# Optimization experiments

Measured on AMD Instinct MI355X. Metric: run time of the kernel, lower is better.

## Reference

```python
import jax, jax.numpy as jnp
import numpy as np

N_NODES = 50000
N_EDGES = 800000
IN_CH = 1024
OUT_CH = 256


def setup_inputs() -> dict:
    key = jax.random.key(0)
    ks = jax.random.split(key, 7)
    x = jax.random.normal(ks[0], (N_NODES, IN_CH), dtype=jnp.float32)
    src_index = jax.random.randint(ks[1], (N_EDGES,), 0, N_NODES, dtype=jnp.int32)
    tar_index = jax.random.randint(ks[2], (N_EDGES,), 0, N_NODES, dtype=jnp.int32)
    edge_weight = jax.random.uniform(ks[3], (N_EDGES,), dtype=jnp.float32)
    self_edge_weight = jax.random.uniform(ks[4], (N_NODES,), dtype=jnp.float32)
    # Linear layer params (torch.nn.Linear: y = x @ W.T + b)
    bound = 1.0 / np.sqrt(IN_CH)
    W = jax.random.uniform(ks[5], (OUT_CH, IN_CH), dtype=jnp.float32, minval=-bound, maxval=bound)
    b = jax.random.uniform(ks[6], (OUT_CH,), dtype=jnp.float32, minval=-bound, maxval=bound)
    return {"x": x, "W": W, "b": b, "src_index": src_index, "tar_index": tar_index,
            "edge_weight": edge_weight, "self_edge_weight": self_edge_weight}


def reference(x, W, b, src_index, tar_index, edge_weight, self_edge_weight):
    # dense linear projection: [N, in] -> [N, out]
    h = jnp.einsum('ni,oi->no', x, W) + b
    # edge aggregation: out[t] += w_e * h[src_e]  (SpMM-like gather/scatter)
    msgs = h[src_index] * edge_weight[:, None]          # [E, out]
    agg = jax.ops.segment_sum(msgs, tar_index, num_segments=h.shape[0])
    # self-loop term
    return agg + self_edge_weight[:, None] * h
```

## Files before the change

### kernel.cpp

```cpp
#include <hip/hip_runtime.h>
#include <hip/hip_bf16.h>

#define N_NODES 50000
#define N_EDGES 800000
#define IN_CH 1024
#define OUT_CH 256
#define NBLK 196

typedef __attribute__((ext_vector_type(8))) short bf16x8;
typedef __attribute__((ext_vector_type(4))) float f32x4;

__device__ inline unsigned short f2bf(float f) {
  union { float f; unsigned int u; } v; v.f = f;
  unsigned int r = v.u + 0x7fffu + ((v.u >> 16) & 1u);
  return (unsigned short)(r >> 16);
}
__device__ inline float bf2f(unsigned short u) {
  union { unsigned int u; float f; } v; v.u = ((unsigned int)u) << 16;
  return v.f;
}
__device__ inline unsigned int cvtpk_bf16(float a, float b) {
  unsigned int r;
  asm("v_cvt_pk_bf16_f32 %0, %1, %2" : "=v"(r) : "v"(a), "v"(b));
  return r;
}

__global__ __launch_bounds__(256) void prep_hist(const float* __restrict__ W,
                                                 unsigned short* __restrict__ Wb,
                                                 const int* __restrict__ tar,
                                                 int* __restrict__ counts) {
  const int b = blockIdx.x, t = threadIdx.x;
  if (b < 256) {
    const int i4 = (b * 256 + t) * 4;
    float4 f = *(const float4*)(W + i4);
    *(ushort4*)(Wb + i4) = make_ushort4(f2bf(f.x), f2bf(f.y), f2bf(f.z), f2bf(f.w));
  } else {
    const int e = (b - 256) * 256 + t;
    if (e < N_EDGES) atomicAdd(&counts[tar[e]], 1);
  }
}

__global__ __launch_bounds__(256, 3) void gemm_proj(
    const float* __restrict__ X, const unsigned short* __restrict__ Wb,
    const float* __restrict__ bias, unsigned short* __restrict__ Hb)
{
  __shared__ unsigned short lds_a[2][64][32];
  __shared__ unsigned short lds_b[2][128][32];

  const int tid  = threadIdx.x;
  const int lane = tid & 63;
  const int w    = tid >> 6;
  const int wr   = w >> 1, wc = w & 1;
  const int gm0  = blockIdx.x * 64;
  const int gn0  = blockIdx.y * 128;

  const int ar = tid >> 3;
  const int ac = (tid & 7) * 4;
  const int br = tid >> 2;
  const int bc = (tid & 3) * 8;

  const int arow0 = gm0 + ar, arow1 = gm0 + ar + 32;
  const bool aok0 = arow0 < N_NODES, aok1 = arow1 < N_NODES;
  const float* xp0 = X + (size_t)arow0 * IN_CH + ac;
  const float* xp1 = X + (size_t)arow1 * IN_CH + ac;
  const unsigned short* wp0 = Wb + (size_t)(gn0 + br) * IN_CH + bc;
  const unsigned short* wp1 = Wb + (size_t)(gn0 + br + 64) * IN_CH + bc;

  f32x4 acc[2][4];
  #pragma unroll
  for (int i = 0; i < 2; i++)
    #pragma unroll
    for (int j = 0; j < 4; j++) acc[i][j] = (f32x4)0.0f;

  float4 pa[3][2];
  bf16x8 pb[2][2];

#define LOADA(KS, SL)                                                          \
  {                                                                            \
    const int k0_ = (KS) * 32;                                                 \
    pa[SL][0] = aok0 ? *(const float4*)(xp0 + k0_)                             \
                     : make_float4(0.f, 0.f, 0.f, 0.f);                        \
    pa[SL][1] = aok1 ? *(const float4*)(xp1 + k0_)                             \
                     : make_float4(0.f, 0.f, 0.f, 0.f);                        \
  }
#define LOADB(KS, SL)                                                          \
  {                                                                            \
    const int k0_ = (KS) * 32;                                                 \
    pb[SL][0] = *(const bf16x8*)(wp0 + k0_);                                   \
    pb[SL][1] = *(const bf16x8*)(wp1 + k0_);                                   \
  }
#define WRITER(BUF, SA, SB)                                                    \
  {                                                                            \
    *(uint2*)&lds_a[BUF][ar][ac] =                                             \
        make_uint2(cvtpk_bf16(pa[SA][0].x, pa[SA][0].y),                       \
                   cvtpk_bf16(pa[SA][0].z, pa[SA][0].w));                      \
    *(uint2*)&lds_a[BUF][ar + 32][ac] =                                        \
        make_uint2(cvtpk_bf16(pa[SA][1].x, pa[SA][1].y),                       \
                   cvtpk_bf16(pa[SA][1].z, pa[SA][1].w));                      \
    *(bf16x8*)&lds_b[BUF][br][bc]      = pb[SB][0];                            \
    *(bf16x8*)&lds_b[BUF][br + 64][bc] = pb[SB][1];                            \
  }
#define COMPUTE(BUF)                                                           \
  {                                                                            \
    const int l15_ = lane & 15;                                                \
    const int kb_  = (lane >> 4) * 8;                                          \
    bf16x8 a0 = *(const bf16x8*)&lds_a[BUF][wr * 32 + l15_][kb_];              \
    bf16x8 a1 = *(const bf16x8*)&lds_a[BUF][wr * 32 + 16 + l15_][kb_];         \
    bf16x8 b0 = *(const bf16x8*)&lds_b[BUF][wc * 64 + l15_][kb_];              \
    bf16x8 b1 = *(const bf16x8*)&lds_b[BUF][wc * 64 + 16 + l15_][kb_];         \
    bf16x8 b2 = *(const bf16x8*)&lds_b[BUF][wc * 64 + 32 + l15_][kb_];         \
    bf16x8 b3 = *(const bf16x8*)&lds_b[BUF][wc * 64 + 48 + l15_][kb_];         \
    acc[0][0] = __builtin_amdgcn_mfma_f32_16x16x32_bf16(a0, b0, acc[0][0], 0, 0, 0); \
    acc[0][1] = __builtin_amdgcn_mfma_f32_16x16x32_bf16(a0, b1, acc[0][1], 0, 0, 0); \
    acc[0][2] = __builtin_amdgcn_mfma_f32_16x16x32_bf16(a0, b2, acc[0][2], 0, 0, 0); \
    acc[0][3] = __builtin_amdgcn_mfma_f32_16x16x32_bf16(a0, b3, acc[0][3], 0, 0, 0); \
    acc[1][0] = __builtin_amdgcn_mfma_f32_16x16x32_bf16(a1, b0, acc[1][0], 0, 0, 0); \
    acc[1][1] = __builtin_amdgcn_mfma_f32_16x16x32_bf16(a1, b1, acc[1][1], 0, 0, 0); \
    acc[1][2] = __builtin_amdgcn_mfma_f32_16x16x32_bf16(a1, b2, acc[1][2], 0, 0, 0); \
    acc[1][3] = __builtin_amdgcn_mfma_f32_16x16x32_bf16(a1, b3, acc[1][3], 0, 0, 0); \
  }

  LOADA(0, 0); LOADA(1, 1); LOADA(2, 2);
  LOADB(0, 0); LOADB(1, 1);
  WRITER(0, 0, 0);
  __syncthreads();

  #pragma unroll
  for (int ks = 0; ks < 32; ks++) {
    if (ks + 3 < 32) LOADA(ks + 3, (ks + 3) % 3);
    if (ks + 2 < 32) LOADB(ks + 2, ks & 1);
    COMPUTE(ks & 1);
    if (ks + 1 < 32) WRITER((ks + 1) & 1, (ks + 1) % 3, (ks + 1) & 1);
    __syncthreads();
  }
#undef LOADA
#undef LOADB
#undef WRITER
#undef COMPUTE

  float bj[4];
  #pragma unroll
  for (int j = 0; j < 4; j++)
    bj[j] = bias[gn0 + wc * 64 + j * 16 + (lane & 15)];

  #pragma unroll
  for (int i = 0; i < 2; i++) {
    const int grow_base = gm0 + wr * 32 + i * 16 + ((lane >> 4) << 2);
    #pragma unroll
    for (int r = 0; r < 4; r++) {
      const int grow = grow_base + r;
      if (grow < N_NODES) {
        #pragma unroll
        for (int j = 0; j < 4; j++) {
          const int gcol = gn0 + wc * 64 + j * 16 + (lane & 15);
          Hb[(size_t)grow * OUT_CH + gcol] = f2bf(acc[i][j][r] + bj[j]);
        }
      }
    }
  }
}

__global__ __launch_bounds__(256) void scan_block(const int* __restrict__ counts,
                                                  int* __restrict__ offsets,
                                                  int* __restrict__ blocksum) {
  __shared__ int wsum[4];
  const int tid = threadIdx.x, lane = tid & 63, wv = tid >> 6;
  const int i = blockIdx.x * 256 + tid;
  const int v = (i < N_NODES) ? counts[i] : 0;
  int s = v;
  #pragma unroll
  for (int off = 1; off < 64; off <<= 1) {
    int t = __shfl_up(s, off, 64);
    if (lane >= off) s += t;
  }
  if (lane == 63) wsum[wv] = s;
  __syncthreads();
  if (tid == 0) {
    int c = 0;
    #pragma unroll
    for (int k = 0; k < 4; k++) { int t = wsum[k]; wsum[k] = c; c += t; }
  }
  __syncthreads();
  const int excl = wsum[wv] + s - v;
  if (i < N_NODES) offsets[i] = excl;
  if (tid == 255) blocksum[blockIdx.x] = excl + v;
}

__global__ __launch_bounds__(256) void scan_sums(int* __restrict__ blocksum,
                                                 int* __restrict__ offsets) {
  __shared__ int wsum[4];
  const int tid = threadIdx.x, lane = tid & 63, wv = tid >> 6;
  const int v = (tid < NBLK) ? blocksum[tid] : 0;
  int s = v;
  #pragma unroll
  for (int off = 1; off < 64; off <<= 1) {
    int t = __shfl_up(s, off, 64);
    if (lane >= off) s += t;
  }
  if (lane == 63) wsum[wv] = s;
  __syncthreads();
  if (tid == 0) {
    int c = 0;
    #pragma unroll
    for (int k = 0; k < 4; k++) { int t = wsum[k]; wsum[k] = c; c += t; }
  }
  __syncthreads();
  const int excl = wsum[wv] + s - v;
  if (tid < NBLK) blocksum[tid] = excl;
  if (tid == 255) offsets[N_NODES] = excl;
}

__global__ __launch_bounds__(256) void finalize_offsets(int* __restrict__ offsets,
                                                        const int* __restrict__ blocksum,
                                                        int* __restrict__ cursor) {
  const int i = blockIdx.x * 256 + threadIdx.x;
  if (i < N_NODES) {
    const int off = offsets[i] + blocksum[i >> 8];
    offsets[i] = off;
    cursor[i] = off;
  }
}

__global__ __launch_bounds__(256) void fill_csr(const int* __restrict__ src,
                                                const int* __restrict__ tar,
                                                const float* __restrict__ ew,
                                                int* __restrict__ cursor,
                                                int2* __restrict__ edata) {
  int e = blockIdx.x * blockDim.x + threadIdx.x;
  if (e >= N_EDGES) return;
  const int t = tar[e];
  const int p = atomicAdd(&cursor[t], 1);
  edata[p] = make_int2(src[e], __float_as_int(ew[e]));
}

__global__ __launch_bounds__(256) void node_agg(
    const unsigned short* __restrict__ Hb, const int* __restrict__ offsets,
    const int2* __restrict__ edata, const float* __restrict__ sw,
    float* __restrict__ OUT)
{
  const int wid = (blockIdx.x * blockDim.x + threadIdx.x) >> 6;
  if (wid >= N_NODES) return;
  const int lane = threadIdx.x & 63;
  const int e0 = offsets[wid];
  const int e1 = offsets[wid + 1];

  float a0 = 0.f, a1 = 0.f, a2 = 0.f, a3 = 0.f;

  for (int base = e0; base < e1; base += 64) {
    const int avail = e1 - base;
    int2 d = make_int2(0, 0);
    if (lane < avail) d = edata[base + lane];
    const int n = (avail < 64) ? avail : 64;
    int j = 0;
    for (; j + 4 <= n; j += 4) {
      const int   s0 = __shfl(d.x, j, 64),     s1 = __shfl(d.x, j + 1, 64);
      const int   s2 = __shfl(d.x, j + 2, 64), s3 = __shfl(d.x, j + 3, 64);
      const float w0 = __int_as_float(__shfl(d.y, j, 64));
      const float w1 = __int_as_float(__shfl(d.y, j + 1, 64));
      const float w2 = __int_as_float(__shfl(d.y, j + 2, 64));
      const float w3 = __int_as_float(__shfl(d.y, j + 3, 64));
      const ushort4 h0 = *(const ushort4*)(Hb + (size_t)s0 * OUT_CH + lane * 4);
      const ushort4 h1 = *(const ushort4*)(Hb + (size_t)s1 * OUT_CH + lane * 4);
      const ushort4 h2 = *(const ushort4*)(Hb + (size_t)s2 * OUT_CH + lane * 4);
      const ushort4 h3 = *(const ushort4*)(Hb + (size_t)s3 * OUT_CH + lane * 4);
      a0 += w0 * bf2f(h0.x) + w1 * bf2f(h1.x) + w2 * bf2f(h2.x) + w3 * bf2f(h3.x);
      a1 += w0 * bf2f(h0.y) + w1 * bf2f(h1.y) + w2 * bf2f(h2.y) + w3 * bf2f(h3.y);
      a2 += w0 * bf2f(h0.z) + w1 * bf2f(h1.z) + w2 * bf2f(h2.z) + w3 * bf2f(h3.z);
      a3 += w0 * bf2f(h0.w) + w1 * bf2f(h1.w) + w2 * bf2f(h2.w) + w3 * bf2f(h3.w);
    }
    for (; j < n; j++) {
      const int   s = __shfl(d.x, j, 64);
      const float wgt = __int_as_float(__shfl(d.y, j, 64));
      const ushort4 h = *(const ushort4*)(Hb + (size_t)s * OUT_CH + lane * 4);
      a0 += wgt * bf2f(h.x); a1 += wgt * bf2f(h.y);
      a2 += wgt * bf2f(h.z); a3 += wgt * bf2f(h.w);
    }
  }

  const float swv = sw[wid];
  const ushort4 hs = *(const ushort4*)(Hb + (size_t)wid * OUT_CH + lane * 4);
  float4 o;
  o.x = a0 + swv * bf2f(hs.x);
  o.y = a1 + swv * bf2f(hs.y);
  o.z = a2 + swv * bf2f(hs.z);
  o.w = a3 + swv * bf2f(hs.w);
  *(float4*)(OUT + (size_t)wid * OUT_CH + lane * 4) = o;
}

extern "C" void kernel_launch(void* const* d_in, const int* in_sizes, int n_in,
                              void* d_out, int out_size, void* d_ws, size_t ws_size,
                              hipStream_t stream) {
  const float* x   = (const float*)d_in[0];
  const float* W   = (const float*)d_in[1];
  const float* b   = (const float*)d_in[2];
  const int*   src = (const int*)d_in[3];
  const int*   tar = (const int*)d_in[4];
  const float* ew  = (const float*)d_in[5];
  const float* sw  = (const float*)d_in[6];
  float* out = (float*)d_out;

  char* ws = (char*)d_ws;
  size_t o = 0;
  unsigned short* Wb = (unsigned short*)(ws + o);
  o += (size_t)OUT_CH * IN_CH * 2;          o = (o + 255) & ~(size_t)255;
  unsigned short* Hb = (unsigned short*)(ws + o);
  o += (size_t)N_NODES * OUT_CH * 2;        o = (o + 255) & ~(size_t)255;
  int* counts   = (int*)(ws + o); o += (size_t)N_NODES * 4;       o = (o + 255) & ~(size_t)255;
  int* offsets  = (int*)(ws + o); o += (size_t)(N_NODES + 1) * 4; o = (o + 255) & ~(size_t)255;
  int* cursor   = (int*)(ws + o); o += (size_t)N_NODES * 4;       o = (o + 255) & ~(size_t)255;
  int* blocksum = (int*)(ws + o); o += (size_t)NBLK * 4;          o = (o + 255) & ~(size_t)255;
  int2* edata   = (int2*)(ws + o);

  hipMemsetAsync(counts, 0, (size_t)N_NODES * 4, stream);
  prep_hist<<<256 + (N_EDGES + 255) / 256, 256, 0, stream>>>(W, Wb, tar, counts);
  scan_block<<<NBLK, 256, 0, stream>>>(counts, offsets, blocksum);
  scan_sums<<<1, 256, 0, stream>>>(blocksum, offsets);
  finalize_offsets<<<NBLK, 256, 0, stream>>>(offsets, blocksum, cursor);
  fill_csr<<<(N_EDGES + 255) / 256, 256, 0, stream>>>(src, tar, ew, cursor, edata);

  dim3 g1((N_NODES + 63) / 64, OUT_CH / 128);
  gemm_proj<<<g1, 256, 0, stream>>>(x, Wb, b, Hb);

  const long long nthreads = (long long)N_NODES * 64;
  node_agg<<<(int)((nthreads + 255) / 256), 256, 0, stream>>>(Hb, offsets, edata, sw, out);
}
```

Baseline: 236.3 us.

## Restructure projection GEMM to stage W in LDS and stream X into registers

The GEMM now loads a 64-column slice of the bf16 weight into a 64KB swizzled LDS buffer in two 512-wide K chunks. Each wave reads its own rows of fp32 X straight from global memory into registers, converts them to bf16 in place, and feeds the MFMA without an LDS round trip. The tile becomes 128x64 with 4 N-blocks instead of 2, so X is read from global four times instead of twice. The goal is to drop the per-k-step LDS writes and barriers for A. The cost is more X traffic, only a one-step register prefetch, a lower occupancy target, and uncoalesced per-lane X loads.

```diff
diff --git a/kernel.cpp b/kernel.cpp
--- a/kernel.cpp
+++ b/kernel.cpp
@@ -40,120 +40,104 @@
   }
 }
 
-__global__ __launch_bounds__(256, 3) void gemm_proj(
+__global__ __launch_bounds__(256, 2) void gemm_proj(
     const float* __restrict__ X, const unsigned short* __restrict__ Wb,
     const float* __restrict__ bias, unsigned short* __restrict__ Hb)
 {
-  __shared__ unsigned short lds_a[2][64][32];
-  __shared__ unsigned short lds_b[2][128][32];
+  __shared__ unsigned short lds_w[64][512];
 
   const int tid  = threadIdx.x;
   const int lane = tid & 63;
-  const int w    = tid >> 6;
-  const int wr   = w >> 1, wc = w & 1;
-  const int gm0  = blockIdx.x * 64;
-  const int gn0  = blockIdx.y * 128;
-
-  const int ar = tid >> 3;
-  const int ac = (tid & 7) * 4;
-  const int br = tid >> 2;
-  const int bc = (tid & 3) * 8;
-
-  const int arow0 = gm0 + ar, arow1 = gm0 + ar + 32;
-  const bool aok0 = arow0 < N_NODES, aok1 = arow1 < N_NODES;
-  const float* xp0 = X + (size_t)arow0 * IN_CH + ac;
-  const float* xp1 = X + (size_t)arow1 * IN_CH + ac;
-  const unsigned short* wp0 = Wb + (size_t)(gn0 + br) * IN_CH + bc;
-  const unsigned short* wp1 = Wb + (size_t)(gn0 + br + 64) * IN_CH + bc;
+  const int wv   = tid >> 6;
+  const int l15  = lane & 15;
+  const int hi   = lane >> 4;
+  const int m0   = blockIdx.x * 128;
+  const int n0   = blockIdx.y * 64;
 
   f32x4 acc[2][4];
   #pragma unroll
-  for (int i = 0; i < 2; i++)
-    #pragma unroll
-    for (int j = 0; j < 4; j++) acc[i][j] = (f32x4)0.0f;
-
-  float4 pa[3][2];
-  bf16x8 pb[2][2];
-
-#define LOADA(KS, SL)                                                          \
-  {                                                                            \
-    const int k0_ = (KS) * 32;                                                 \
-    pa[SL][0] = aok0 ? *(const float4*)(xp0 + k0_)                             \
-                     : make_float4(0.f, 0.f, 0.f, 0.f);                        \
-    pa[SL][1] = aok1 ? *(const float4*)(xp1 + k0_)                             \
-                     : make_float4(0.f, 0.f, 0.f, 0.f);                        \
-  }
-#define LOADB(KS, SL)                                                          \
-  {                                                                            \
-    const int k0_ = (KS) * 32;                                                 \
-    pb[SL][0] = *(const bf16x8*)(wp0 + k0_);                                   \
-    pb[SL][1] = *(const bf16x8*)(wp1 + k0_);                                   \
-  }
-#define WRITER(BUF, SA, SB)                                                    \
-  {                                                                            \
-    *(uint2*)&lds_a[BUF][ar][ac] =                                             \
-        make_uint2(cvtpk_bf16(pa[SA][0].x, pa[SA][0].y),                       \
-                   cvtpk_bf16(pa[SA][0].z, pa[SA][0].w));                      \
-    *(uint2*)&lds_a[BUF][ar + 32][ac] =                                        \
-        make_uint2(cvtpk_bf16(pa[SA][1].x, pa[SA][1].y),                       \
-                   cvtpk_bf16(pa[SA][1].z, pa[SA][1].w));                      \
-    *(bf16x8*)&lds_b[BUF][br][bc]      = pb[SB][0];                            \
-    *(bf16x8*)&lds_b[BUF][br + 64][bc] = pb[SB][1];                            \
-  }
-#define COMPUTE(BUF)                                                           \
-  {                                                                            \
-    const int l15_ = lane & 15;                                                \
-    const int kb_  = (lane >> 4) * 8;                                          \
-    bf16x8 a0 = *(const bf16x8*)&lds_a[BUF][wr * 32 + l15_][kb_];              \
-    bf16x8 a1 = *(const bf16x8*)&lds_a[BUF][wr * 32 + 16 + l15_][kb_];         \
-    bf16x8 b0 = *(const bf16x8*)&lds_b[BUF][wc * 64 + l15_][kb_];              \
-    bf16x8 b1 = *(const bf16x8*)&lds_b[BUF][wc * 64 + 16 + l15_][kb_];         \
-    bf16x8 b2 = *(const bf16x8*)&lds_b[BUF][wc * 64 + 32 + l15_][kb_];         \
-    bf16x8 b3 = *(const bf16x8*)&lds_b[BUF][wc * 64 + 48 + l15_][kb_];         \
-    acc[0][0] = __builtin_amdgcn_mfma_f32_16x16x32_bf16(a0, b0, acc[0][0], 0, 0, 0); \
-    acc[0][1] = __builtin_amdgcn_mfma_f32_16x16x32_bf16(a0, b1, acc[0][1], 0, 0, 0); \
-    acc[0][2] = __builtin_amdgcn_mfma_f32_16x16x32_bf16(a0, b2, acc[0][2], 0, 0, 0); \
-    acc[0][3] = __builtin_amdgcn_mfma_f32_16x16x32_bf16(a0, b3, acc[0][3], 0, 0, 0); \
-    acc[1][0] = __builtin_amdgcn_mfma_f32_16x16x32_bf16(a1, b0, acc[1][0], 0, 0, 0); \
-    acc[1][1] = __builtin_amdgcn_mfma_f32_16x16x32_bf16(a1, b1, acc[1][1], 0, 0, 0); \
-    acc[1][2] = __builtin_amdgcn_mfma_f32_16x16x32_bf16(a1, b2, acc[1][2], 0, 0, 0); \
-    acc[1][3] = __builtin_amdgcn_mfma_f32_16x16x32_bf16(a1, b3, acc[1][3], 0, 0, 0); \
-  }
-
-  LOADA(0, 0); LOADA(1, 1); LOADA(2, 2);
-  LOADB(0, 0); LOADB(1, 1);
-  WRITER(0, 0, 0);
-  __syncthreads();
-
-  #pragma unroll
-  for (int ks = 0; ks < 32; ks++) {
-    if (ks + 3 < 32) LOADA(ks + 3, (ks + 3) % 3);
-    if (ks + 2 < 32) LOADB(ks + 2, ks & 1);
-    COMPUTE(ks & 1);
-    if (ks + 1 < 32) WRITER((ks + 1) & 1, (ks + 1) % 3, (ks + 1) & 1);
+  for (int f = 0; f < 2; f++)
+    #pragma unroll
+    for (int j = 0; j < 4; j++) acc[f][j] = (f32x4)0.0f;
+
+  const int r0 = m0 + wv * 32 + l15;
+  const int r1 = r0 + 16;
+  const bool ok0 = r0 < N_NODES, ok1 = r1 < N_NODES;
+  const float* xa0 = X + (size_t)r0 * IN_CH + hi * 8;
+  const float* xa1 = X + (size_t)r1 * IN_CH + hi * 8;
+  const float4 fz = make_float4(0.f, 0.f, 0.f, 0.f);
+
+  for (int kc = 0; kc < 2; kc++) {
+    if (kc) __syncthreads();
+    #pragma unroll
+    for (int it = 0; it < 16; it++) {
+      const int idx = it * 256 + tid;
+      const int n   = idx >> 6;
+      const int c   = idx & 63;
+      const int pc  = c ^ (n & 7);
+      const bf16x8 v =
+          *(const bf16x8*)(Wb + (size_t)(n0 + n) * IN_CH + kc * 512 + c * 8);
+      *(bf16x8*)&lds_w[n][pc * 8] = v;
+    }
     __syncthreads();
-  }
-#undef LOADA
-#undef LOADB
-#undef WRITER
-#undef COMPUTE
+
+    const int kbase = kc * 512;
+    float4 nA0a, nA0b, nA1a, nA1b;
+    nA0a = ok0 ? *(const float4*)(xa0 + kbase)     : fz;
+    nA0b = ok0 ? *(const float4*)(xa0 + kbase + 4) : fz;
+    nA1a = ok1 ? *(const float4*)(xa1 + kbase)     : fz;
+    nA1b = ok1 ? *(const float4*)(xa1 + kbase + 4) : fz;
+
+    #pragma unroll
+    for (int ks = 0; ks < 16; ks++) {
+      const float4 cA0a = nA0a, cA0b = nA0b, cA1a = nA1a, cA1b = nA1b;
+      if (ks + 1 < 16) {
+        const int ko = kbase + (ks + 1) * 32;
+        nA0a = ok0 ? *(const float4*)(xa0 + ko)     : fz;
+        nA0b = ok0 ? *(const float4*)(xa0 + ko + 4) : fz;
+        nA1a = ok1 ? *(const float4*)(xa1 + ko)     : fz;
+        nA1b = ok1 ? *(const float4*)(xa1 + ko + 4) : fz;
+      }
+      const int pc = ((ks << 2) + hi) ^ (l15 & 7);
+      const bf16x8 bf0 = *(const bf16x8*)&lds_w[l15][pc * 8];
+      const bf16x8 bf1 = *(const bf16x8*)&lds_w[16 + l15][pc * 8];
+      const bf16x8 bf2 = *(const bf16x8*)&lds_w[32 + l15][pc * 8];
+      const bf16x8 bf3 = *(const bf16x8*)&lds_w[48 + l15][pc * 8];
+      union { unsigned int u[4]; bf16x8 v; } t0, t1;
+      t0.u[0] = cvtpk_bf16(cA0a.x, cA0a.y);
+      t0.u[1] = cvtpk_bf16(cA0a.z, cA0a.w);
+      t0.u[2] = cvtpk_bf16(cA0b.x, cA0b.y);
+      t0.u[3] = cvtpk_bf16(cA0b.z, cA0b.w);
+      t1.u[0] = cvtpk_bf16(cA1a.x, cA1a.y);
+      t1.u[1] = cvtpk_bf16(cA1a.z, cA1a.w);
+      t1.u[2] = cvtpk_bf16(cA1b.x, cA1b.y);
+      t1.u[3] = cvtpk_bf16(cA1b.z, cA1b.w);
+      acc[0][0] = __builtin_amdgcn_mfma_f32_16x16x32_bf16(t0.v, bf0, acc[0][0], 0, 0, 0);
+      acc[0][1] = __builtin_amdgcn_mfma_f32_16x16x32_bf16(t0.v, bf1, acc[0][1], 0, 0, 0);
+      acc[0][2] = __builtin_amdgcn_mfma_f32_16x16x32_bf16(t0.v, bf2, acc[0][2], 0, 0, 0);
+      acc[0][3] = __builtin_amdgcn_mfma_f32_16x16x32_bf16(t0.v, bf3, acc[0][3], 0, 0, 0);
+      acc[1][0] = __builtin_amdgcn_mfma_f32_16x16x32_bf16(t1.v, bf0, acc[1][0], 0, 0, 0);
+      acc[1][1] = __builtin_amdgcn_mfma_f32_16x16x32_bf16(t1.v, bf1, acc[1][1], 0, 0, 0);
+      acc[1][2] = __builtin_amdgcn_mfma_f32_16x16x32_bf16(t1.v, bf2, acc[1][2], 0, 0, 0);
+      acc[1][3] = __builtin_amdgcn_mfma_f32_16x16x32_bf16(t1.v, bf3, acc[1][3], 0, 0, 0);
+    }
+  }
 
   float bj[4];
   #pragma unroll
-  for (int j = 0; j < 4; j++)
-    bj[j] = bias[gn0 + wc * 64 + j * 16 + (lane & 15)];
-
-  #pragma unroll
-  for (int i = 0; i < 2; i++) {
-    const int grow_base = gm0 + wr * 32 + i * 16 + ((lane >> 4) << 2);
+  for (int j = 0; j < 4; j++) bj[j] = bias[n0 + 16 * j + l15];
+
+  #pragma unroll
+  for (int f = 0; f < 2; f++) {
+    const int grow_base = m0 + wv * 32 + f * 16 + hi * 4;
     #pragma unroll
     for (int r = 0; r < 4; r++) {
       const int grow = grow_base + r;
       if (grow < N_NODES) {
         #pragma unroll
         for (int j = 0; j < 4; j++) {
-          const int gcol = gn0 + wc * 64 + j * 16 + (lane & 15);
-          Hb[(size_t)grow * OUT_CH + gcol] = f2bf(acc[i][j][r] + bj[j]);
+          const int gcol = n0 + 16 * j + l15;
+          Hb[(size_t)grow * OUT_CH + gcol] = f2bf(acc[f][j][r] + bj[j]);
         }
       }
     }
@@ -318,7 +302,7 @@
   finalize_offsets<<<NBLK, 256, 0, stream>>>(offsets, blocksum, cursor);
   fill_csr<<<(N_EDGES + 255) / 256, 256, 0, stream>>>(src, tar, ew, cursor, edata);
 
-  dim3 g1((N_NODES + 63) / 64, OUT_CH / 128);
+  dim3 g1((N_NODES + 127) / 128, OUT_CH / 64);
   gemm_proj<<<g1, 256, 0, stream>>>(x, Wb, b, Hb);
 
   const long long nthreads = (long long)N_NODES * 64;
```

New measurement: 567.3 us. +140.1%, slower.
